# Optimization experiments

Hardware: AMD Instinct MI355X
Metric: run time of the kernel (lower is better)

The kernel has to match this reference:

```python
import jax, jax.numpy as jnp
import numpy as np

N_NODES = 50000
N_EDGES = 800000
IN_CH = 128
HID = 128
OUT_CH = 1
N_GRAPHS = 256


def setup_inputs() -> dict:
    key = jax.random.key(0)
    ks = jax.random.split(key, 12)
    x = jax.random.normal(ks[0], (N_NODES, IN_CH), dtype=jnp.float32)
    edge_index = jax.random.randint(ks[1], (2, N_EDGES), 0, N_NODES, dtype=jnp.int64)
    batch = jnp.sort(jax.random.randint(ks[2], (N_NODES,), 0, N_GRAPHS, dtype=jnp.int64))
    s1 = 1.0 / np.sqrt(IN_CH)
    s2 = 1.0 / np.sqrt(HID)
    W1 = jax.random.uniform(ks[3], (IN_CH, HID), jnp.float32, -s1, s1)
    b1 = jax.random.uniform(ks[4], (HID,), jnp.float32, -s1, s1)
    W2 = jax.random.uniform(ks[5], (HID, HID), jnp.float32, -s2, s2)
    b2 = jax.random.uniform(ks[6], (HID,), jnp.float32, -s2, s2)
    Wl1 = jax.random.uniform(ks[7], (HID, HID), jnp.float32, -s2, s2)
    bl1 = jax.random.uniform(ks[8], (HID,), jnp.float32, -s2, s2)
    Wl2 = jax.random.uniform(ks[9], (HID, OUT_CH), jnp.float32, -s2, s2)
    bl2 = jax.random.uniform(ks[10], (OUT_CH,), jnp.float32, -s2, s2)
    return {"x": x, "edge_index": edge_index, "batch": batch,
            "W1": W1, "b1": b1, "W2": W2, "b2": b2,
            "Wl1": Wl1, "bl1": bl1, "Wl2": Wl2, "bl2": bl2}


def gcn_conv(x, src, dst, W, b, n_nodes):
    # PyG GCNConv: h = X W; add self-loops; sym-normalized scatter-add; + bias
    h = x @ W                                     # [N, H]
    deg = jax.ops.segment_sum(jnp.ones_like(dst, dtype=h.dtype), dst, n_nodes)
    dinv = jnp.where(deg > 0, jax.lax.rsqrt(deg), 0.0)
    norm = dinv[src] * dinv[dst]                  # [E+N]
    msg = h[src] * norm[:, None]                  # gather [E+N, H]
    return jax.ops.segment_sum(msg, dst, n_nodes) + b


def reference(x, edge_index, batch, W1, b1, W2, b2, Wl1, bl1, Wl2, bl2):
    n_nodes = x.shape[0]
    loops = jnp.arange(n_nodes, dtype=edge_index.dtype)
    src = jnp.concatenate([edge_index[0], loops])
    dst = jnp.concatenate([edge_index[1], loops])
    h = jax.nn.relu(gcn_conv(x, src, dst, W1, b1, n_nodes))
    h = jax.nn.relu(gcn_conv(h, src, dst, W2, b2, n_nodes))
    # global mean pool over graphs
    sums = jax.ops.segment_sum(h, batch, N_GRAPHS)                 # [G, H]
    cnt = jax.ops.segment_sum(jnp.ones((n_nodes,), h.dtype), batch, N_GRAPHS)
    g = sums / jnp.maximum(cnt, 1.0)[:, None]
    g = jax.nn.relu(g @ Wl1 + bl1)
    return g @ Wl2 + bl2                                           # [G, 1]
```

## Files before the change

### kernel.cpp

```cpp
#include <hip/hip_runtime.h>

#define NN 50000
#define NE 800000
#define HD 128
#define NG 256
#define ELLW 64
#define NBUCK 196
#define BCAP 4736
#define CSTRIDE 16
#define EPT 8
#define EPB (256 * EPT)
#define NB_GEMM ((NN + 63) / 64)
#define NB_SCAT ((NE + EPB - 1) / EPB)

__device__ __forceinline__ unsigned f32_to_bf16_rne(float f) {
  unsigned u = __float_as_uint(f);
  return (u + 0x7fffu + ((u >> 16) & 1u)) >> 16;
}

__device__ __forceinline__ void gemm_tile(const float* xs, const float* __restrict__ W,
                                          const int* __restrict__ deg, ushort* __restrict__ out,
                                          int row0, int t, bool scale) {
  int lane = t & 31;
  int rg = t >> 5;
  const float4* W4 = (const float4*)W;
  float acc[8][4] = {};
#pragma unroll 2
  for (int k = 0; k < 128; k += 4) {
    float4 b[4];
#pragma unroll
    for (int kk = 0; kk < 4; ++kk) b[kk] = W4[(size_t)(k + kk) * 32 + lane];
    float4 a[8];
#pragma unroll
    for (int i = 0; i < 8; ++i) a[i] = *(const float4*)&xs[(rg * 8 + i) * 128 + k];
#pragma unroll
    for (int i = 0; i < 8; ++i) {
      acc[i][0] = fmaf(a[i].x, b[0].x, acc[i][0]);
      acc[i][1] = fmaf(a[i].x, b[0].y, acc[i][1]);
      acc[i][2] = fmaf(a[i].x, b[0].z, acc[i][2]);
      acc[i][3] = fmaf(a[i].x, b[0].w, acc[i][3]);
      acc[i][0] = fmaf(a[i].y, b[1].x, acc[i][0]);
      acc[i][1] = fmaf(a[i].y, b[1].y, acc[i][1]);
      acc[i][2] = fmaf(a[i].y, b[1].z, acc[i][2]);
      acc[i][3] = fmaf(a[i].y, b[1].w, acc[i][3]);
      acc[i][0] = fmaf(a[i].z, b[2].x, acc[i][0]);
      acc[i][1] = fmaf(a[i].z, b[2].y, acc[i][1]);
      acc[i][2] = fmaf(a[i].z, b[2].z, acc[i][2]);
      acc[i][3] = fmaf(a[i].z, b[2].w, acc[i][3]);
      acc[i][0] = fmaf(a[i].w, b[3].x, acc[i][0]);
      acc[i][1] = fmaf(a[i].w, b[3].y, acc[i][1]);
      acc[i][2] = fmaf(a[i].w, b[3].z, acc[i][2]);
      acc[i][3] = fmaf(a[i].w, b[3].w, acc[i][3]);
    }
  }
#pragma unroll
  for (int i = 0; i < 8; ++i) {
    int r = row0 + rg * 8 + i;
    if (r < NN) {
      float d = scale ? rsqrtf((float)(deg[r] + 1)) : 1.0f;
      ushort4 o;
      o.x = (ushort)f32_to_bf16_rne(acc[i][0] * d);
      o.y = (ushort)f32_to_bf16_rne(acc[i][1] * d);
      o.z = (ushort)f32_to_bf16_rne(acc[i][2] * d);
      o.w = (ushort)f32_to_bf16_rne(acc[i][3] * d);
      *(ushort4*)&out[(size_t)r * 128 + lane * 4] = o;
    }
  }
}

__global__ __launch_bounds__(256) void scatter_gemm_k(const float* __restrict__ X, const float* __restrict__ W1,
                                                      ushort* __restrict__ tmp,
                                                      const int* __restrict__ src, const int* __restrict__ dst,
                                                      int* __restrict__ cursor, uint* __restrict__ ebuf) {
  __shared__ __align__(16) char smem[32768];
  int t = threadIdx.x;
  if (blockIdx.x < NB_GEMM) {
    float* xs = (float*)smem;
    int row0 = blockIdx.x * 64;
    const float4* X4 = (const float4*)X;
    float4* xs4 = (float4*)xs;
#pragma unroll
    for (int i = 0; i < 8; ++i) {
      int idx = i * 256 + t;
      int r = row0 + (idx >> 5);
      if (r > NN - 1) r = NN - 1;
      xs4[idx] = X4[(size_t)r * 32 + (idx & 31)];
    }
    __syncthreads();
    gemm_tile(xs, W1, nullptr, tmp, row0, t, false);
  } else {
    uint*   stage   = (uint*)smem;
    uint*   payload = (uint*)(smem + 8192);
    uint*   meta    = (uint*)(smem + 16384);
    unsigned char* sbuck = (unsigned char*)(smem + 24576);
    int*    bcnt  = (int*)(smem + 26624);
    int*    scan  = (int*)(smem + 27648);
    int*    boff  = (int*)(smem + 28672);
    int*    gbase = (int*)(smem + 29696);
    bcnt[t] = 0;
    __syncthreads();
    int base = (blockIdx.x - NB_GEMM) * EPB + t;
#pragma unroll 4
    for (int k = 0; k < EPT; ++k) {
      int e = base + k * 256;
      if (e < NE) {
        int d = dst[e];
        int s = src[e];
        int bk = d >> 8;
        int lp = atomicAdd(&bcnt[bk], 1);
        payload[k * 256 + t] = ((uint)s << 8) | (uint)(d & 255);
        meta[k * 256 + t] = ((uint)bk << 16) | (uint)lp;
      }
    }
    __syncthreads();
    int v = bcnt[t];
    scan[t] = v;
    __syncthreads();
    for (int off = 1; off < 256; off <<= 1) {
      int x = (t >= off) ? scan[t - off] : 0;
      __syncthreads();
      scan[t] += x;
      __syncthreads();
    }
    boff[t] = scan[t] - v;
    if (t < NBUCK && v > 0) gbase[t] = atomicAdd(&cursor[t * CSTRIDE], v);
    __syncthreads();
#pragma unroll 4
    for (int k = 0; k < EPT; ++k) {
      int e = base + k * 256;
      if (e < NE) {
        uint m = meta[k * 256 + t];
        int bk = (int)(m >> 16);
        int lp = (int)(m & 0xffffu);
        int slot = boff[bk] + lp;
        stage[slot] = payload[k * 256 + t];
        sbuck[slot] = (unsigned char)bk;
      }
    }
    __syncthreads();
    int ntot = scan[255];
    for (int i = t; i < ntot; i += 256) {
      int b = sbuck[i];
      int pos = gbase[b] + (i - boff[b]);
      if (pos < BCAP) ebuf[(size_t)b * BCAP + pos] = stage[i];
    }
  }
}

__global__ __launch_bounds__(256) void ellbuild_k(const int* __restrict__ cursor, const uint* __restrict__ ebuf,
                                                  const int* __restrict__ batch,
                                                  int* __restrict__ deg, ushort* __restrict__ ell,
                                                  int* __restrict__ gstart, int* __restrict__ gend) {
  __shared__ ushort lell[256 * ELLW];
  __shared__ int lcnt[256];
  int t = threadIdx.x;
  int b = blockIdx.x;
  lcnt[t] = 0;
  __syncthreads();
  int ne = cursor[b * CSTRIDE];
  if (ne > BCAP) ne = BCAP;
  for (int i = t; i < ne; i += 256) {
    uint u = ebuf[(size_t)b * BCAP + i];
    int dl = u & 255;
    int p = atomicAdd(&lcnt[dl], 1);
    if (p < ELLW) lell[dl * ELLW + p] = (ushort)(u >> 8);
  }
  __syncthreads();
  int node = b * 256 + t;
  if (node < NN) {
    deg[node] = lcnt[t];
    int g = batch[node];
    if (node == 0 || batch[node - 1] != g) gstart[g] = node;
    if (node == NN - 1 || batch[node + 1] != g) gend[g] = node + 1;
  }
  const uint* l4 = (const uint*)lell;
  uint* g4 = (uint*)ell;
  for (int idx = t; idx < 256 * 32; idx += 256) {
    int nod = b * 256 + (idx >> 5);
    if (nod < NN) g4[(size_t)nod * 32 + (idx & 31)] = l4[idx];
  }
}

__global__ __launch_bounds__(256) void gemm128_k(const ushort* __restrict__ H, const float* __restrict__ W,
                                                 const int* __restrict__ deg, ushort* __restrict__ out) {
  __shared__ float xs[64 * 128];
  int t = threadIdx.x;
  int row0 = blockIdx.x * 64;
  const uint* H2 = (const uint*)H;
#pragma unroll
  for (int i = 0; i < 16; ++i) {
    int idx = i * 256 + t;
    int r = row0 + (idx >> 6);
    if (r > NN - 1) r = NN - 1;
    int c = idx & 63;
    uint u = H2[(size_t)r * 64 + c];
    float2 f;
    f.x = __uint_as_float(u << 16);
    f.y = __uint_as_float(u & 0xffff0000u);
    *(float2*)&xs[(idx >> 6) * 128 + c * 2] = f;
  }
  __syncthreads();
  gemm_tile(xs, W, deg, out, row0, t, true);
}

template <bool POOL, bool SSRC>
__global__ __launch_bounds__(256) void aggregate_k(const ushort* __restrict__ tmp2,
                                                   const ushort* __restrict__ ell, const int* __restrict__ deg,
                                                   const float* __restrict__ bias,
                                                   ushort* __restrict__ out,
                                                   const int* __restrict__ batch, float* __restrict__ sums) {
  int wid = threadIdx.x >> 6;
  int lane = threadIdx.x & 63;
  int n = blockIdx.x * 4 + wid;
  if (n >= NN) return;
  const uint* TU = (const uint*)tmp2;
  int dn = deg[n];
  float dv = rsqrtf((float)(dn + 1));
  uint sv = TU[(size_t)n * 64 + lane];
  float sw = SSRC ? dv : 1.0f;
  float2 acc;
  acc.x = __uint_as_float(sv << 16) * sw;
  acc.y = __uint_as_float(sv & 0xffff0000u) * sw;
  int d = dn; if (d > ELLW) d = ELLW;
  int idx = (int)ell[(size_t)n * ELLW + lane];
  int j = 0;
  for (; j + 8 <= d; j += 8) {
    int s0 = __shfl(idx, j);
    int s1 = __shfl(idx, j + 1);
    int s2 = __shfl(idx, j + 2);
    int s3 = __shfl(idx, j + 3);
    int s4 = __shfl(idx, j + 4);
    int s5 = __shfl(idx, j + 5);
    int s6 = __shfl(idx, j + 6);
    int s7 = __shfl(idx, j + 7);
    float d0 = SSRC ? rsqrtf((float)(deg[s0] + 1)) : 1.0f;
    float d1 = SSRC ? rsqrtf((float)(deg[s1] + 1)) : 1.0f;
    float d2 = SSRC ? rsqrtf((float)(deg[s2] + 1)) : 1.0f;
    float d3 = SSRC ? rsqrtf((float)(deg[s3] + 1)) : 1.0f;
    float d4 = SSRC ? rsqrtf((float)(deg[s4] + 1)) : 1.0f;
    float d5 = SSRC ? rsqrtf((float)(deg[s5] + 1)) : 1.0f;
    float d6 = SSRC ? rsqrtf((float)(deg[s6] + 1)) : 1.0f;
    float d7 = SSRC ? rsqrtf((float)(deg[s7] + 1)) : 1.0f;
    uint v0 = TU[(size_t)s0 * 64 + lane];
    uint v1 = TU[(size_t)s1 * 64 + lane];
    uint v2 = TU[(size_t)s2 * 64 + lane];
    uint v3 = TU[(size_t)s3 * 64 + lane];
    uint v4 = TU[(size_t)s4 * 64 + lane];
    uint v5 = TU[(size_t)s5 * 64 + lane];
    uint v6 = TU[(size_t)s6 * 64 + lane];
    uint v7 = TU[(size_t)s7 * 64 + lane];
    if (SSRC) {
      acc.x = fmaf(__uint_as_float(v0 << 16), d0, acc.x);
      acc.y = fmaf(__uint_as_float(v0 & 0xffff0000u), d0, acc.y);
      acc.x = fmaf(__uint_as_float(v1 << 16), d1, acc.x);
      acc.y = fmaf(__uint_as_float(v1 & 0xffff0000u), d1, acc.y);
      acc.x = fmaf(__uint_as_float(v2 << 16), d2, acc.x);
      acc.y = fmaf(__uint_as_float(v2 & 0xffff0000u), d2, acc.y);
      acc.x = fmaf(__uint_as_float(v3 << 16), d3, acc.x);
      acc.y = fmaf(__uint_as_float(v3 & 0xffff0000u), d3, acc.y);
      acc.x = fmaf(__uint_as_float(v4 << 16), d4, acc.x);
      acc.y = fmaf(__uint_as_float(v4 & 0xffff0000u), d4, acc.y);
      acc.x = fmaf(__uint_as_float(v5 << 16), d5, acc.x);
      acc.y = fmaf(__uint_as_float(v5 & 0xffff0000u), d5, acc.y);
      acc.x = fmaf(__uint_as_float(v6 << 16), d6, acc.x);
      acc.y = fmaf(__uint_as_float(v6 & 0xffff0000u), d6, acc.y);
      acc.x = fmaf(__uint_as_float(v7 << 16), d7, acc.x);
      acc.y = fmaf(__uint_as_float(v7 & 0xffff0000u), d7, acc.y);
    } else {
      float x0 = __uint_as_float(v0 << 16), y0 = __uint_as_float(v0 & 0xffff0000u);
      float x1 = __uint_as_float(v1 << 16), y1 = __uint_as_float(v1 & 0xffff0000u);
      float x2 = __uint_as_float(v2 << 16), y2 = __uint_as_float(v2 & 0xffff0000u);
      float x3 = __uint_as_float(v3 << 16), y3 = __uint_as_float(v3 & 0xffff0000u);
      float x4 = __uint_as_float(v4 << 16), y4 = __uint_as_float(v4 & 0xffff0000u);
      float x5 = __uint_as_float(v5 << 16), y5 = __uint_as_float(v5 & 0xffff0000u);
      float x6 = __uint_as_float(v6 << 16), y6 = __uint_as_float(v6 & 0xffff0000u);
      float x7 = __uint_as_float(v7 << 16), y7 = __uint_as_float(v7 & 0xffff0000u);
      acc.x += ((x0 + x1) + (x2 + x3)) + ((x4 + x5) + (x6 + x7));
      acc.y += ((y0 + y1) + (y2 + y3)) + ((y4 + y5) + (y6 + y7));
    }
  }
  for (; j < d; ++j) {
    int s0 = __shfl(idx, j);
    float d0 = SSRC ? rsqrtf((float)(deg[s0] + 1)) : 1.0f;
    uint v = TU[(size_t)s0 * 64 + lane];
    acc.x = fmaf(__uint_as_float(v << 16), d0, acc.x);
    acc.y = fmaf(__uint_as_float(v & 0xffff0000u), d0, acc.y);
  }
  float2 bb = ((const float2*)bias)[lane];
  float ox = fmaxf(fmaf(acc.x, dv, bb.x), 0.0f);
  float oy = fmaxf(fmaf(acc.y, dv, bb.y), 0.0f);
  if (POOL) {
    int g = batch[n];
    float* sp = &sums[(size_t)g * HD + lane * 2];
    atomicAdd(sp + 0, ox);
    atomicAdd(sp + 1, oy);
  } else {
    uint pk = f32_to_bf16_rne(ox) | (f32_to_bf16_rne(oy) << 16);
    ((uint*)out)[(size_t)n * 64 + lane] = pk;
  }
}

__global__ __launch_bounds__(128) void mlp_k(const float* __restrict__ sums,
                                             const int* __restrict__ gstart, const int* __restrict__ gend,
                                             const float* __restrict__ Wl1, const float* __restrict__ bl1,
                                             const float* __restrict__ Wl2, const float* __restrict__ bl2,
                                             float* __restrict__ out) {
  __shared__ float gs[128];
  __shared__ float red[128];
  int g = blockIdx.x, t = threadIdx.x;
  int c = gend[g] - gstart[g]; if (c < 1) c = 1;
  gs[t] = sums[(size_t)g * HD + t] / (float)c;
  __syncthreads();
  float acc = bl1[t];
#pragma unroll 8
  for (int k = 0; k < 128; ++k) acc = fmaf(gs[k], Wl1[k * HD + t], acc);
  acc = fmaxf(acc, 0.0f);
  red[t] = acc * Wl2[t];
  __syncthreads();
  for (int off = 64; off > 0; off >>= 1) {
    if (t < off) red[t] += red[t + off];
    __syncthreads();
  }
  if (t == 0) out[g] = red[0] + bl2[0];
}

extern "C" void kernel_launch(void* const* d_in, const int* in_sizes, int n_in,
                              void* d_out, int out_size, void* d_ws, size_t ws_size,
                              hipStream_t stream) {
  const float* x   = (const float*)d_in[0];
  const int*   edge = (const int*)d_in[1];
  const int*   batch = (const int*)d_in[2];
  const float* W1  = (const float*)d_in[3];
  const float* b1  = (const float*)d_in[4];
  const float* W2  = (const float*)d_in[5];
  const float* b2  = (const float*)d_in[6];
  const float* Wl1 = (const float*)d_in[7];
  const float* bl1 = (const float*)d_in[8];
  const float* Wl2 = (const float*)d_in[9];
  const float* bl2 = (const float*)d_in[10];
  const int* srcp = edge;
  const int* dstp = edge + NE;

  char* w = (char*)d_ws;
  size_t off = 0;
  auto alloc = [&](size_t bytes) -> void* {
    void* p = w + off;
    off += (bytes + 255) & ~(size_t)255;
    return p;
  };
  int*    cursor = (int*)alloc((size_t)NBUCK * CSTRIDE * 4);
  int*    gstart = (int*)alloc(NG * 4);
  int*    gend   = (int*)alloc(NG * 4);
  float*  sums   = (float*)alloc((size_t)NG * HD * 4);
  size_t zero_bytes = off;
  int*    deg  = (int*)alloc(NN * 4);
  uint*   ebuf = (uint*)alloc((size_t)NBUCK * BCAP * 4);
  ushort* ell  = (ushort*)alloc((size_t)NN * ELLW * 2);
  ushort* tmp  = (ushort*)alloc((size_t)NN * HD * 2);
  ushort* h1   = (ushort*)alloc((size_t)NN * HD * 2);
  ushort* tmp2 = (ushort*)alloc((size_t)NN * HD * 2);

  hipMemsetAsync(cursor, 0, zero_bytes, stream);

  scatter_gemm_k<<<NB_GEMM + NB_SCAT, 256, 0, stream>>>(x, W1, tmp, srcp, dstp, cursor, ebuf);
  ellbuild_k<<<NBUCK, 256, 0, stream>>>(cursor, ebuf, batch, deg, ell, gstart, gend);
  aggregate_k<false, true><<<(NN + 3) / 4, 256, 0, stream>>>(tmp, ell, deg, b1, h1, nullptr, nullptr);
  gemm128_k<<<(NN + 63) / 64, 256, 0, stream>>>(h1, W2, deg, tmp2);
  aggregate_k<true, false><<<(NN + 3) / 4, 256, 0, stream>>>(tmp2, ell, deg, b2, nullptr, batch, sums);
  mlp_k<<<NG, 128, 0, stream>>>(sums, gstart, gend, Wl1, bl1, Wl2, bl2, (float*)d_out);
}
```

Baseline: 181.2 us.

## Split feature matrices into column halves and aggregate each half separately

The GEMM outputs are now stored as two contiguous column-half arrays of 64 bf16 features (128 bytes per node) instead of full 256-byte rows. Each aggregation runs as two launches, one per half, and each wave uses its two 32-lane halves to gather two neighbours at once, combined with a cross-half shuffle at the end. The aim is a smaller gather working set per pass, so it fits better in cache, and more neighbour rows in flight per wave. The cost is two extra kernel launches, duplicated index and degree loads per half, and a GEMM store pattern split across two arrays.

```diff
diff --git a/kernel.cpp b/kernel.cpp
--- a/kernel.cpp
+++ b/kernel.cpp
@@ -12,6 +12,7 @@
 #define EPB (256 * EPT)
 #define NB_GEMM ((NN + 63) / 64)
 #define NB_SCAT ((NE + EPB - 1) / EPB)
+#define HALFU ((size_t)NN * 32)
 
 __device__ __forceinline__ unsigned f32_to_bf16_rne(float f) {
   unsigned u = __float_as_uint(f);
@@ -19,7 +20,7 @@
 }
 
 __device__ __forceinline__ void gemm_tile(const float* xs, const float* __restrict__ W,
-                                          const int* __restrict__ deg, ushort* __restrict__ out,
+                                          const int* __restrict__ deg, uint* __restrict__ outU,
                                           int row0, int t, bool scale) {
   int lane = t & 31;
   int rg = t >> 5;
@@ -58,18 +59,18 @@
     int r = row0 + rg * 8 + i;
     if (r < NN) {
       float d = scale ? rsqrtf((float)(deg[r] + 1)) : 1.0f;
-      ushort4 o;
-      o.x = (ushort)f32_to_bf16_rne(acc[i][0] * d);
-      o.y = (ushort)f32_to_bf16_rne(acc[i][1] * d);
-      o.z = (ushort)f32_to_bf16_rne(acc[i][2] * d);
-      o.w = (ushort)f32_to_bf16_rne(acc[i][3] * d);
-      *(ushort4*)&out[(size_t)r * 128 + lane * 4] = o;
+      uint u0 = f32_to_bf16_rne(acc[i][0] * d) | (f32_to_bf16_rne(acc[i][1] * d) << 16);
+      uint u1 = f32_to_bf16_rne(acc[i][2] * d) | (f32_to_bf16_rne(acc[i][3] * d) << 16);
+      size_t hoff = (lane < 16) ? 0 : HALFU;
+      uint* p = outU + hoff + (size_t)r * 32 + ((2 * lane) & 31);
+      p[0] = u0;
+      p[1] = u1;
     }
   }
 }
 
 __global__ __launch_bounds__(256) void scatter_gemm_k(const float* __restrict__ X, const float* __restrict__ W1,
-                                                      ushort* __restrict__ tmp,
+                                                      uint* __restrict__ tmp,
                                                       const int* __restrict__ src, const int* __restrict__ dst,
                                                       int* __restrict__ cursor, uint* __restrict__ ebuf) {
   __shared__ __align__(16) char smem[32768];
@@ -181,19 +182,18 @@
   }
 }
 
-__global__ __launch_bounds__(256) void gemm128_k(const ushort* __restrict__ H, const float* __restrict__ W,
-                                                 const int* __restrict__ deg, ushort* __restrict__ out) {
+__global__ __launch_bounds__(256) void gemm128_k(const uint* __restrict__ H, const float* __restrict__ W,
+                                                 const int* __restrict__ deg, uint* __restrict__ out) {
   __shared__ float xs[64 * 128];
   int t = threadIdx.x;
   int row0 = blockIdx.x * 64;
-  const uint* H2 = (const uint*)H;
 #pragma unroll
   for (int i = 0; i < 16; ++i) {
     int idx = i * 256 + t;
     int r = row0 + (idx >> 6);
     if (r > NN - 1) r = NN - 1;
     int c = idx & 63;
-    uint u = H2[(size_t)r * 64 + c];
+    uint u = H[(size_t)r * 64 + c];
     float2 f;
     f.x = __uint_as_float(u << 16);
     f.y = __uint_as_float(u & 0xffff0000u);
@@ -204,68 +204,78 @@
 }
 
 template <bool POOL, bool SSRC>
-__global__ __launch_bounds__(256) void aggregate_k(const ushort* __restrict__ tmp2,
+__global__ __launch_bounds__(256) void aggregate_k(const uint* __restrict__ TU,
                                                    const ushort* __restrict__ ell, const int* __restrict__ deg,
                                                    const float* __restrict__ bias,
-                                                   ushort* __restrict__ out,
-                                                   const int* __restrict__ batch, float* __restrict__ sums) {
+                                                   uint* __restrict__ outU,
+                                                   const int* __restrict__ batch, float* __restrict__ sums,
+                                                   int hf) {
   int wid = threadIdx.x >> 6;
   int lane = threadIdx.x & 63;
+  int half = lane >> 5;
+  int col = lane & 31;
   int n = blockIdx.x * 4 + wid;
   if (n >= NN) return;
-  const uint* TU = (const uint*)tmp2;
   int dn = deg[n];
   float dv = rsqrtf((float)(dn + 1));
-  uint sv = TU[(size_t)n * 64 + lane];
-  float sw = SSRC ? dv : 1.0f;
+  uint sv = TU[(size_t)n * 32 + col];
+  float sw = half ? 0.0f : (SSRC ? dv : 1.0f);
   float2 acc;
   acc.x = __uint_as_float(sv << 16) * sw;
   acc.y = __uint_as_float(sv & 0xffff0000u) * sw;
   int d = dn; if (d > ELLW) d = ELLW;
   int idx = (int)ell[(size_t)n * ELLW + lane];
   int j = 0;
-  for (; j + 8 <= d; j += 8) {
-    int s0 = __shfl(idx, j);
-    int s1 = __shfl(idx, j + 1);
-    int s2 = __shfl(idx, j + 2);
-    int s3 = __shfl(idx, j + 3);
-    int s4 = __shfl(idx, j + 4);
-    int s5 = __shfl(idx, j + 5);
-    int s6 = __shfl(idx, j + 6);
-    int s7 = __shfl(idx, j + 7);
-    float d0 = SSRC ? rsqrtf((float)(deg[s0] + 1)) : 1.0f;
-    float d1 = SSRC ? rsqrtf((float)(deg[s1] + 1)) : 1.0f;
-    float d2 = SSRC ? rsqrtf((float)(deg[s2] + 1)) : 1.0f;
-    float d3 = SSRC ? rsqrtf((float)(deg[s3] + 1)) : 1.0f;
-    float d4 = SSRC ? rsqrtf((float)(deg[s4] + 1)) : 1.0f;
-    float d5 = SSRC ? rsqrtf((float)(deg[s5] + 1)) : 1.0f;
-    float d6 = SSRC ? rsqrtf((float)(deg[s6] + 1)) : 1.0f;
-    float d7 = SSRC ? rsqrtf((float)(deg[s7] + 1)) : 1.0f;
-    uint v0 = TU[(size_t)s0 * 64 + lane];
-    uint v1 = TU[(size_t)s1 * 64 + lane];
-    uint v2 = TU[(size_t)s2 * 64 + lane];
-    uint v3 = TU[(size_t)s3 * 64 + lane];
-    uint v4 = TU[(size_t)s4 * 64 + lane];
-    uint v5 = TU[(size_t)s5 * 64 + lane];
-    uint v6 = TU[(size_t)s6 * 64 + lane];
-    uint v7 = TU[(size_t)s7 * 64 + lane];
+  for (; j + 16 <= d; j += 16) {
+    int s0 = __shfl(idx, j),      s1 = __shfl(idx, j + 1);
+    int s2 = __shfl(idx, j + 2),  s3 = __shfl(idx, j + 3);
+    int s4 = __shfl(idx, j + 4),  s5 = __shfl(idx, j + 5);
+    int s6 = __shfl(idx, j + 6),  s7 = __shfl(idx, j + 7);
+    int s8 = __shfl(idx, j + 8),  s9 = __shfl(idx, j + 9);
+    int sa = __shfl(idx, j + 10), sb = __shfl(idx, j + 11);
+    int sc = __shfl(idx, j + 12), sd = __shfl(idx, j + 13);
+    int se = __shfl(idx, j + 14), sf = __shfl(idx, j + 15);
+    int a0 = half ? s1 : s0;
+    int a1 = half ? s3 : s2;
+    int a2 = half ? s5 : s4;
+    int a3 = half ? s7 : s6;
+    int a4 = half ? s9 : s8;
+    int a5 = half ? sb : sa;
+    int a6 = half ? sd : sc;
+    int a7 = half ? sf : se;
+    uint v0 = TU[(size_t)a0 * 32 + col];
+    uint v1 = TU[(size_t)a1 * 32 + col];
+    uint v2 = TU[(size_t)a2 * 32 + col];
+    uint v3 = TU[(size_t)a3 * 32 + col];
+    uint v4 = TU[(size_t)a4 * 32 + col];
+    uint v5 = TU[(size_t)a5 * 32 + col];
+    uint v6 = TU[(size_t)a6 * 32 + col];
+    uint v7 = TU[(size_t)a7 * 32 + col];
     if (SSRC) {
-      acc.x = fmaf(__uint_as_float(v0 << 16), d0, acc.x);
-      acc.y = fmaf(__uint_as_float(v0 & 0xffff0000u), d0, acc.y);
-      acc.x = fmaf(__uint_as_float(v1 << 16), d1, acc.x);
-      acc.y = fmaf(__uint_as_float(v1 & 0xffff0000u), d1, acc.y);
-      acc.x = fmaf(__uint_as_float(v2 << 16), d2, acc.x);
-      acc.y = fmaf(__uint_as_float(v2 & 0xffff0000u), d2, acc.y);
-      acc.x = fmaf(__uint_as_float(v3 << 16), d3, acc.x);
-      acc.y = fmaf(__uint_as_float(v3 & 0xffff0000u), d3, acc.y);
-      acc.x = fmaf(__uint_as_float(v4 << 16), d4, acc.x);
-      acc.y = fmaf(__uint_as_float(v4 & 0xffff0000u), d4, acc.y);
-      acc.x = fmaf(__uint_as_float(v5 << 16), d5, acc.x);
-      acc.y = fmaf(__uint_as_float(v5 & 0xffff0000u), d5, acc.y);
-      acc.x = fmaf(__uint_as_float(v6 << 16), d6, acc.x);
-      acc.y = fmaf(__uint_as_float(v6 & 0xffff0000u), d6, acc.y);
-      acc.x = fmaf(__uint_as_float(v7 << 16), d7, acc.x);
-      acc.y = fmaf(__uint_as_float(v7 & 0xffff0000u), d7, acc.y);
+      float e0 = half ? rsqrtf((float)(deg[s1] + 1)) : rsqrtf((float)(deg[s0] + 1));
+      float e1 = half ? rsqrtf((float)(deg[s3] + 1)) : rsqrtf((float)(deg[s2] + 1));
+      float e2 = half ? rsqrtf((float)(deg[s5] + 1)) : rsqrtf((float)(deg[s4] + 1));
+      float e3 = half ? rsqrtf((float)(deg[s7] + 1)) : rsqrtf((float)(deg[s6] + 1));
+      float e4 = half ? rsqrtf((float)(deg[s9] + 1)) : rsqrtf((float)(deg[s8] + 1));
+      float e5 = half ? rsqrtf((float)(deg[sb] + 1)) : rsqrtf((float)(deg[sa] + 1));
+      float e6 = half ? rsqrtf((float)(deg[sd] + 1)) : rsqrtf((float)(deg[sc] + 1));
+      float e7 = half ? rsqrtf((float)(deg[sf] + 1)) : rsqrtf((float)(deg[se] + 1));
+      acc.x = fmaf(__uint_as_float(v0 << 16), e0, acc.x);
+      acc.y = fmaf(__uint_as_float(v0 & 0xffff0000u), e0, acc.y);
+      acc.x = fmaf(__uint_as_float(v1 << 16), e1, acc.x);
+      acc.y = fmaf(__uint_as_float(v1 & 0xffff0000u), e1, acc.y);
+      acc.x = fmaf(__uint_as_float(v2 << 16), e2, acc.x);
+      acc.y = fmaf(__uint_as_float(v2 & 0xffff0000u), e2, acc.y);
+      acc.x = fmaf(__uint_as_float(v3 << 16), e3, acc.x);
+      acc.y = fmaf(__uint_as_float(v3 & 0xffff0000u), e3, acc.y);
+      acc.x = fmaf(__uint_as_float(v4 << 16), e4, acc.x);
+      acc.y = fmaf(__uint_as_float(v4 & 0xffff0000u), e4, acc.y);
+      acc.x = fmaf(__uint_as_float(v5 << 16), e5, acc.x);
+      acc.y = fmaf(__uint_as_float(v5 & 0xffff0000u), e5, acc.y);
+      acc.x = fmaf(__uint_as_float(v6 << 16), e6, acc.x);
+      acc.y = fmaf(__uint_as_float(v6 & 0xffff0000u), e6, acc.y);
+      acc.x = fmaf(__uint_as_float(v7 << 16), e7, acc.x);
+      acc.y = fmaf(__uint_as_float(v7 & 0xffff0000u), e7, acc.y);
     } else {
       float x0 = __uint_as_float(v0 << 16), y0 = __uint_as_float(v0 & 0xffff0000u);
       float x1 = __uint_as_float(v1 << 16), y1 = __uint_as_float(v1 & 0xffff0000u);
@@ -279,24 +289,38 @@
       acc.y += ((y0 + y1) + (y2 + y3)) + ((y4 + y5) + (y6 + y7));
     }
   }
-  for (; j < d; ++j) {
+  for (; j + 2 <= d; j += 2) {
+    int s0 = __shfl(idx, j), s1 = __shfl(idx, j + 1);
+    int a = half ? s1 : s0;
+    uint v = TU[(size_t)a * 32 + col];
+    float e;
+    if (SSRC) e = half ? rsqrtf((float)(deg[s1] + 1)) : rsqrtf((float)(deg[s0] + 1));
+    else e = 1.0f;
+    acc.x = fmaf(__uint_as_float(v << 16), e, acc.x);
+    acc.y = fmaf(__uint_as_float(v & 0xffff0000u), e, acc.y);
+  }
+  if (j < d) {
     int s0 = __shfl(idx, j);
-    float d0 = SSRC ? rsqrtf((float)(deg[s0] + 1)) : 1.0f;
-    uint v = TU[(size_t)s0 * 64 + lane];
-    acc.x = fmaf(__uint_as_float(v << 16), d0, acc.x);
-    acc.y = fmaf(__uint_as_float(v & 0xffff0000u), d0, acc.y);
-  }
-  float2 bb = ((const float2*)bias)[lane];
+    uint v = TU[(size_t)s0 * 32 + col];
+    float e;
+    if (SSRC) e = half ? 0.0f : rsqrtf((float)(deg[s0] + 1));
+    else e = half ? 0.0f : 1.0f;
+    acc.x = fmaf(__uint_as_float(v << 16), e, acc.x);
+    acc.y = fmaf(__uint_as_float(v & 0xffff0000u), e, acc.y);
+  }
+  acc.x += __shfl_xor(acc.x, 32);
+  acc.y += __shfl_xor(acc.y, 32);
+  if (half) return;
+  float2 bb = ((const float2*)bias)[hf * 32 + col];
   float ox = fmaxf(fmaf(acc.x, dv, bb.x), 0.0f);
   float oy = fmaxf(fmaf(acc.y, dv, bb.y), 0.0f);
   if (POOL) {
     int g = batch[n];
-    float* sp = &sums[(size_t)g * HD + lane * 2];
+    float* sp = &sums[(size_t)g * HD + hf * 64 + col * 2];
     atomicAdd(sp + 0, ox);
     atomicAdd(sp + 1, oy);
   } else {
-    uint pk = f32_to_bf16_rne(ox) | (f32_to_bf16_rne(oy) << 16);
-    ((uint*)out)[(size_t)n * 64 + lane] = pk;
+    outU[(size_t)n * 64 + hf * 32 + col] = f32_to_bf16_rne(ox) | (f32_to_bf16_rne(oy) << 16);
   }
 }
 
@@ -356,16 +380,19 @@
   int*    deg  = (int*)alloc(NN * 4);
   uint*   ebuf = (uint*)alloc((size_t)NBUCK * BCAP * 4);
   ushort* ell  = (ushort*)alloc((size_t)NN * ELLW * 2);
-  ushort* tmp  = (ushort*)alloc((size_t)NN * HD * 2);
-  ushort* h1   = (ushort*)alloc((size_t)NN * HD * 2);
-  ushort* tmp2 = (ushort*)alloc((size_t)NN * HD * 2);
+  uint*   tmp  = (uint*)alloc(HALFU * 2 * 4);
+  uint*   h1   = (uint*)alloc((size_t)NN * 64 * 4);
+  uint*   tmp2 = (uint*)alloc(HALFU * 2 * 4);
+  float*  sumsp = sums;
 
   hipMemsetAsync(cursor, 0, zero_bytes, stream);
 
   scatter_gemm_k<<<NB_GEMM + NB_SCAT, 256, 0, stream>>>(x, W1, tmp, srcp, dstp, cursor, ebuf);
   ellbuild_k<<<NBUCK, 256, 0, stream>>>(cursor, ebuf, batch, deg, ell, gstart, gend);
-  aggregate_k<false, true><<<(NN + 3) / 4, 256, 0, stream>>>(tmp, ell, deg, b1, h1, nullptr, nullptr);
+  aggregate_k<false, true><<<(NN + 3) / 4, 256, 0, stream>>>(tmp, ell, deg, b1, h1, nullptr, nullptr, 0);
+  aggregate_k<false, true><<<(NN + 3) / 4, 256, 0, stream>>>(tmp + HALFU, ell, deg, b1, h1, nullptr, nullptr, 1);
   gemm128_k<<<(NN + 63) / 64, 256, 0, stream>>>(h1, W2, deg, tmp2);
-  aggregate_k<true, false><<<(NN + 3) / 4, 256, 0, stream>>>(tmp2, ell, deg, b2, nullptr, batch, sums);
+  aggregate_k<true, false><<<(NN + 3) / 4, 256, 0, stream>>>(tmp2, ell, deg, b2, nullptr, batch, sumsp, 0);
+  aggregate_k<true, false><<<(NN + 3) / 4, 256, 0, stream>>>(tmp2 + HALFU, ell, deg, b2, nullptr, batch, sumsp, 1);
   mlp_k<<<NG, 128, 0, stream>>>(sums, gstart, gend, Wl1, bl1, Wl2, bl2, (float*)d_out);
 }
```

Measured after the change: 255.4 us. +40.9%, slower.
